# Kernel optimization log

Hardware: AMD Instinct MI355X
Metric: run time of the kernel (lower is better)

## Reference

```python
import jax, jax.numpy as jnp
import numpy as np

N_NODES = 50000
N_EDGES = 1600000
IN_DIM, HID_DIM, OUT_DIM, HEADS = 128, 128, 64, 8
NEG_SLOPE = 0.2
BN_EPS = 1e-5


def setup_inputs() -> dict:
    key = jax.random.key(0)
    ks = jax.random.split(key, 12)
    hpc = HID_DIM // HEADS  # per-head channels of layer 1
    return {
        "x": jax.random.normal(ks[0], (N_NODES, IN_DIM), jnp.float32),
        "edge_index": jax.random.randint(ks[1], (2, N_EDGES), 0, N_NODES, jnp.int64),
        "W1": jax.random.normal(ks[2], (IN_DIM, HEADS * hpc), jnp.float32) * 0.05,
        "a1_src": jax.random.normal(ks[3], (HEADS, hpc), jnp.float32) * 0.1,
        "a1_dst": jax.random.normal(ks[4], (HEADS, hpc), jnp.float32) * 0.1,
        "b1": jnp.zeros((HEADS * hpc,), jnp.float32),
        "bn_gamma": jnp.ones((HID_DIM,), jnp.float32),
        "bn_beta": jnp.zeros((HID_DIM,), jnp.float32),
        "W2": jax.random.normal(ks[5], (HID_DIM, OUT_DIM), jnp.float32) * 0.05,
        "a2_src": jax.random.normal(ks[6], (1, OUT_DIM), jnp.float32) * 0.1,
        "a2_dst": jax.random.normal(ks[7], (1, OUT_DIM), jnp.float32) * 0.1,
        "b2": jnp.zeros((OUT_DIM,), jnp.float32),
    }


def _gat_conv(x, src, dst, W, a_src, a_dst, bias, heads, n_nodes):
    # x: [N, Fin]; src/dst: [E'] (self-loops already appended)
    hpc = W.shape[1] // heads
    h = (x @ W).reshape(n_nodes, heads, hpc)                 # [N,H,C]
    alpha_s = jnp.einsum("nhc,hc->nh", h, a_src)             # [N,H]
    alpha_d = jnp.einsum("nhc,hc->nh", h, a_dst)
    e = alpha_s[src] + alpha_d[dst]                          # [E',H]
    e = jax.nn.leaky_relu(e, NEG_SLOPE)
    # segment softmax over destination neighborhoods
    m = jax.ops.segment_max(e, dst, num_segments=n_nodes)    # [N,H]
    m = jnp.where(jnp.isfinite(m), m, 0.0)
    ee = jnp.exp(e - m[dst])
    denom = jax.ops.segment_sum(ee, dst, num_segments=n_nodes)
    alpha = ee / (denom[dst] + 1e-16)                        # [E',H]
    msg = h[src] * alpha[:, :, None]                         # [E',H,C]
    out = jax.ops.segment_sum(msg, dst, num_segments=n_nodes)  # [N,H,C]
    return out.reshape(n_nodes, heads * hpc) + bias


def _batch_norm(x, gamma, beta):
    mu = jnp.mean(x, axis=0)
    var = jnp.var(x, axis=0)
    return gamma * (x - mu) * jax.lax.rsqrt(var + BN_EPS) + beta


def reference(x, edge_index, W1, a1_src, a1_dst, b1, bn_gamma, bn_beta, W2, a2_src, a2_dst, b2):
    n = x.shape[0]
    loops = jnp.arange(n, dtype=edge_index.dtype)
    src = jnp.concatenate([edge_index[0], loops])            # PyG add_self_loops
    dst = jnp.concatenate([edge_index[1], loops])
    h = _gat_conv(x, src, dst, W1, a1_src, a1_dst, b1, HEADS, n)
    h = _batch_norm(h, bn_gamma, bn_beta)
    h = jax.nn.elu(h)
    # dropout: identity at inference
    out = _gat_conv(h, src, dst, W2, a2_src, a2_dst, b2, 1, n)
    return out
```

## Files before the change

### kernel.cpp

```cpp
#include <hip/hip_runtime.h>
#include <hip/hip_bf16.h>

#define N_NODES 50000
#define N_EDGES 1600000
#define HEADS 8
#define NBK 196
#define NBLK 196
#define EPB 8192

typedef unsigned short u16;
typedef unsigned char u8;
typedef unsigned int u32;
typedef __attribute__((ext_vector_type(8))) short bf16x8;
typedef __attribute__((ext_vector_type(4))) float f32x4;

__device__ __forceinline__ float bf2f(u16 u) {
  union { u32 i; float f; } v; v.i = ((u32)u) << 16; return v.f;
}
__device__ __forceinline__ float bflo(u32 p) {
  union { u32 i; float f; } v; v.i = p << 16; return v.f;
}
__device__ __forceinline__ float bfhi(u32 p) {
  union { u32 i; float f; } v; v.i = p & 0xffff0000u; return v.f;
}
__device__ __forceinline__ u16 f2bf(float f) {
  union { float f; u32 i; } v; v.f = f;
  u32 r = v.i + 0x7fff + ((v.i >> 16) & 1);
  return (u16)(r >> 16);
}
__device__ __forceinline__ u32 pack2(float a, float b) {
  return (u32)f2bf(a) | ((u32)f2bf(b) << 16);
}

__global__ void k_detect(const u16* __restrict__ x, const u32* __restrict__ ei,
                         int* __restrict__ flags) {
  __shared__ int cbig, cnz;
  if (threadIdx.x == 0) { cbig = 0; cnz = 0; }
  __syncthreads();
  int lb = 0, ln = 0;
  for (int i = threadIdx.x; i < 4096; i += 256) {
    int ex = (x[i] >> 7) & 0xff;
    lb += (ex >= 140);
    if (i < 2048) ln += (ei[2 * i + 1] != 0);
  }
  atomicAdd(&cbig, lb); atomicAdd(&cnz, ln);
  __syncthreads();
  if (threadIdx.x == 0) {
    flags[0] = (cbig > 16) ? 1 : 0;
    flags[1] = (cnz == 0) ? 1 : 0;
  }
}

__global__ void k_convsmall(const void* a1s, const void* a1d, const void* b1,
                            const void* gam, const void* bet, const void* a2s,
                            const void* a2d, const void* b2, const void* W1,
                            const void* W2, float* __restrict__ smallf,
                            u16* __restrict__ w1t, u16* __restrict__ w2t,
                            const int* __restrict__ flags) {
  int i = blockIdx.x * 256 + threadIdx.x;
  if (i >= 25408) return;
  bool f32 = flags[0] != 0;
  auto ld = [&](const void* p, int off) -> float {
    return f32 ? ((const float*)p)[off] : bf2f(((const u16*)p)[off]);
  };
  if (i >= 17216) {
    int j = i - 17216, n = j >> 7, k = j & 127;
    w2t[j] = f2bf(ld(W2, k * 64 + n));
  } else if (i >= 832) {
    int j = i - 832, n = j >> 7, k = j & 127;
    w1t[j] = f2bf(ld(W1, k * 128 + n));
  } else {
    const void* src; int off;
    if (i >= 768)      { src = b2;  off = i - 768; }
    else if (i >= 704) { src = a2d; off = i - 704; }
    else if (i >= 640) { src = a2s; off = i - 640; }
    else if (i >= 512) { src = bet; off = i - 512; }
    else if (i >= 384) { src = gam; off = i - 384; }
    else if (i >= 256) { src = b1;  off = i - 256; }
    else if (i >= 128) { src = a1d; off = i - 128; }
    else               { src = a1s; off = i; }
    smallf[i] = ld(src, off);
  }
}

__global__ __launch_bounds__(256) void k_hist(const int* __restrict__ ei,
                                              int* __restrict__ H,
                                              int* __restrict__ totals,
                                              const int* __restrict__ flags) {
  __shared__ int hist[NBK];
  int t = threadIdx.x, blk = blockIdx.x;
  for (int i = t; i < NBK; i += 256) hist[i] = 0;
  __syncthreads();
  bool i64 = flags[1] != 0;
  int base = blk * EPB;
  for (int k = 0; k < 32; k++) {
    int e = base + k * 256 + t;
    if (e < N_EDGES) {
      int d = i64 ? ei[2 * (N_EDGES + e)] : ei[N_EDGES + e];
      atomicAdd(&hist[d >> 8], 1);
    }
  }
  __syncthreads();
  for (int i = t; i < NBK; i += 256) {
    H[i * NBLK + blk] = hist[i];
    atomicAdd(&totals[i], hist[i]);
  }
}

__global__ void k_scan_tot(const int* __restrict__ totals, int* __restrict__ bucketBase) {
  __shared__ int tmp[256];
  int t = threadIdx.x;
  int v = (t < NBK) ? totals[t] : 0;
  tmp[t] = v; __syncthreads();
  for (int o = 1; o < 256; o <<= 1) {
    int x = (t >= o) ? tmp[t - o] : 0; __syncthreads();
    tmp[t] += x; __syncthreads();
  }
  if (t < NBK) bucketBase[t] = tmp[t] - v;
  if (t == NBK - 1) bucketBase[NBK] = tmp[t];
}

__global__ void k_scan_blk(const int* __restrict__ H, const int* __restrict__ bucketBase,
                           int* __restrict__ P) {
  __shared__ int tmp[256];
  int t = threadIdx.x, b = blockIdx.x;
  int v = (t < NBLK) ? H[b * NBLK + t] : 0;
  tmp[t] = v; __syncthreads();
  for (int o = 1; o < 256; o <<= 1) {
    int x = (t >= o) ? tmp[t - o] : 0; __syncthreads();
    tmp[t] += x; __syncthreads();
  }
  if (t < NBLK) P[b * NBLK + t] = bucketBase[b] + tmp[t] - v;
}

__global__ __launch_bounds__(256) void k_bucket(const int* __restrict__ ei,
                                                const int* __restrict__ P,
                                                u32* __restrict__ buf,
                                                const int* __restrict__ flags) {
  __shared__ u32 sv[EPB];
  __shared__ u16 rank[EPB];
  __shared__ u8  sk8[EPB];
  __shared__ int cnt[NBK], scn[NBK], tmp[256];
  int t = threadIdx.x, blk = blockIdx.x;
  int base = blk * EPB;
  int nE = N_EDGES - base; if (nE > EPB) nE = EPB;
  for (int i = t; i < NBK; i += 256) cnt[i] = 0;
  __syncthreads();
  bool i64 = flags[1] != 0;
  for (int k = 0; k < EPB / 256; k++) {
    int li = k * 256 + t, e = base + li;
    if (li < nE) {
      int d = i64 ? ei[2 * (N_EDGES + e)] : ei[N_EDGES + e];
      rank[li] = (u16)atomicAdd(&cnt[d >> 8], 1);
    }
  }
  __syncthreads();
  int v = (t < NBK) ? cnt[t] : 0;
  tmp[t] = v; __syncthreads();
  for (int o = 1; o < 256; o <<= 1) {
    int x = (t >= o) ? tmp[t - o] : 0; __syncthreads();
    tmp[t] += x; __syncthreads();
  }
  if (t < NBK) scn[t] = tmp[t] - v;
  __syncthreads();
  for (int k = 0; k < EPB / 256; k++) {
    int li = k * 256 + t, e = base + li;
    if (li < nE) {
      int s = i64 ? ei[2 * e] : ei[e];
      int d = i64 ? ei[2 * (N_EDGES + e)] : ei[N_EDGES + e];
      int key = d >> 8;
      int pos = scn[key] + rank[li];
      sv[pos] = ((u32)(d & 255) << 16) | (u32)s;
      sk8[pos] = (u8)key;
    }
  }
  __syncthreads();
  for (int i = t; i < nE; i += 256) {
    int b = sk8[i];
    buf[P[b * NBLK + blk] + (i - scn[b])] = sv[i];
  }
}

__global__ __launch_bounds__(256) void k_csr(const u32* __restrict__ buf,
                                             const int* __restrict__ bucketBase,
                                             int* __restrict__ row_start,
                                             int* __restrict__ deg,
                                             int* __restrict__ csr, int N) {
  __shared__ int cnt[256], scn[256], cur[256];
  int b = blockIdx.x, t = threadIdx.x;
  int lo = bucketBase[b], hi = bucketBase[b + 1];
  cnt[t] = 0; __syncthreads();
  for (int e = lo + t; e < hi; e += 256) atomicAdd(&cnt[(buf[e] >> 16) & 255], 1);
  __syncthreads();
  int v = cnt[t];
  scn[t] = v; __syncthreads();
  for (int o = 1; o < 256; o <<= 1) {
    int x = (t >= o) ? scn[t - o] : 0; __syncthreads();
    scn[t] += x; __syncthreads();
  }
  int excl = scn[t] - v;
  int node = b * 256 + t;
  if (node < N) { row_start[node] = lo + excl; deg[node] = v; }
  cur[t] = lo + excl;
  __syncthreads();
  for (int e = lo + t; e < hi; e += 256) {
    u32 p = buf[e];
    int pos = atomicAdd(&cur[(p >> 16) & 255], 1);
    csr[pos] = p & 0xffff;
  }
}

template <int NCOLS, bool EPI, bool AFLAG>
__global__ __launch_bounds__(256) void k_gemm_mfma(const void* __restrict__ A,
                                                   const u16* __restrict__ BT,
                                                   const float* __restrict__ scale,
                                                   const float* __restrict__ shift,
                                                   const float* __restrict__ a2s,
                                                   const float* __restrict__ a2d,
                                                   float* __restrict__ as_out,
                                                   float* __restrict__ ad_out,
                                                   u16* __restrict__ C, int M,
                                                   const int* __restrict__ flags) {
  constexpr int KP = 136;
  constexpr int NT = NCOLS / 16;
  __shared__ u16 As[64 * KP];
  __shared__ u16 Bs[NCOLS * KP];
  int t = threadIdx.x;
  int row0 = blockIdx.x * 64;
  bool af32 = AFLAG ? (flags[0] != 0) : false;

  for (int i = t; i < NCOLS * 16; i += 256) {
    int n = i >> 4, q = i & 15;
    *(uint4*)&Bs[n * KP + q * 8] = ((const uint4*)BT)[n * 16 + q];
  }
  for (int i = t; i < 64 * 32; i += 256) {
    int r = i >> 5, c4 = i & 31;
    int row = row0 + r;
    uint2 pk = make_uint2(0u, 0u);
    if (row < M) {
      if (EPI) {
        uint2 p = ((const uint2*)A)[(size_t)row * 32 + c4];
        int c = c4 * 4;
        float v0 = bflo(p.x), v1 = bfhi(p.x), v2 = bflo(p.y), v3 = bfhi(p.y);
        v0 = fmaf(v0, scale[c],     shift[c]);     v0 = v0 > 0.f ? v0 : __expf(v0) - 1.f;
        v1 = fmaf(v1, scale[c + 1], shift[c + 1]); v1 = v1 > 0.f ? v1 : __expf(v1) - 1.f;
        v2 = fmaf(v2, scale[c + 2], shift[c + 2]); v2 = v2 > 0.f ? v2 : __expf(v2) - 1.f;
        v3 = fmaf(v3, scale[c + 3], shift[c + 3]); v3 = v3 > 0.f ? v3 : __expf(v3) - 1.f;
        pk.x = pack2(v0, v1); pk.y = pack2(v2, v3);
      } else if (af32) {
        float4 v = ((const float4*)A)[(size_t)row * 32 + c4];
        pk.x = pack2(v.x, v.y); pk.y = pack2(v.z, v.w);
      } else {
        pk = ((const uint2*)A)[(size_t)row * 32 + c4];
      }
    }
    *(uint2*)&As[r * KP + c4 * 4] = pk;
  }
  __syncthreads();

  int lane = t & 63, w = t >> 6;
  int m = lane & 15, quad = lane >> 4;
  f32x4 acc[NT];
#pragma unroll
  for (int nt = 0; nt < NT; nt++) acc[nt] = (f32x4)(0.f);
  const u16* aBase = &As[(w * 16 + m) * KP + quad * 8];
  const u16* bBase = &Bs[m * KP + quad * 8];
#pragma unroll
  for (int ks = 0; ks < 4; ks++) {
    bf16x8 af = *(const bf16x8*)(aBase + ks * 32);
#pragma unroll
    for (int nt = 0; nt < NT; nt++) {
      bf16x8 bf = *(const bf16x8*)(bBase + nt * 16 * KP + ks * 32);
      acc[nt] = __builtin_amdgcn_mfma_f32_16x16x32_bf16(af, bf, acc[nt], 0, 0, 0);
    }
  }
  int orow0 = row0 + w * 16 + quad * 4;
#pragma unroll
  for (int nt = 0; nt < NT; nt++) {
#pragma unroll
    for (int r = 0; r < 4; r++) {
      int row = orow0 + r;
      if (row < M) C[(size_t)row * NCOLS + nt * 16 + m] = f2bf(acc[nt][r]);
    }
  }
  if (EPI) {
    float a2sv[NT], a2dv[NT];
#pragma unroll
    for (int nt = 0; nt < NT; nt++) { a2sv[nt] = a2s[nt * 16 + m]; a2dv[nt] = a2d[nt * 16 + m]; }
#pragma unroll
    for (int r = 0; r < 4; r++) {
      float vs = 0.f, vd = 0.f;
#pragma unroll
      for (int nt = 0; nt < NT; nt++) {
        vs = fmaf(acc[nt][r], a2sv[nt], vs);
        vd = fmaf(acc[nt][r], a2dv[nt], vd);
      }
      vs += __shfl_xor(vs, 1); vd += __shfl_xor(vd, 1);
      vs += __shfl_xor(vs, 2); vd += __shfl_xor(vd, 2);
      vs += __shfl_xor(vs, 4); vd += __shfl_xor(vd, 4);
      vs += __shfl_xor(vs, 8); vd += __shfl_xor(vd, 8);
      int row = orow0 + r;
      if (row < M && m == 0) { as_out[row] = vs; ad_out[row] = vd; }
    }
  }
}

__global__ void k_alpha1(const u16* __restrict__ h1b, const float* __restrict__ a1s,
                         const float* __restrict__ a1d, float* __restrict__ as_out,
                         float* __restrict__ ad_out, int N) {
  int idx = blockIdx.x * 256 + threadIdx.x;
  if (idx >= N * HEADS) return;
  int n = idx >> 3, h = idx & 7;
  const u32* hp = (const u32*)&h1b[((size_t)n << 7) + (h << 4)];
  float s = 0.f, d = 0.f;
#pragma unroll
  for (int q = 0; q < 8; q++) {
    u32 p = hp[q];
    float v0 = bflo(p), v1 = bfhi(p);
    int b = (h << 4) + q * 2;
    s = fmaf(v0, a1s[b], s); s = fmaf(v1, a1s[b + 1], s);
    d = fmaf(v0, a1d[b], d); d = fmaf(v1, a1d[b + 1], d);
  }
  as_out[idx] = s; ad_out[idx] = d;
}

__global__ __launch_bounds__(256) void k_agg1(const u16* __restrict__ h1b,
                                              const float* __restrict__ as_,
                                              const float* __restrict__ ad_,
                                              const int* __restrict__ csr,
                                              const int* __restrict__ row_start,
                                              const int* __restrict__ deg,
                                              const float* __restrict__ b1,
                                              u16* __restrict__ out, int N) {
  int node = blockIdx.x * 4 + (threadIdx.x >> 6);
  if (node >= N) return;
  int l = threadIdx.x & 63;
  int head = l >> 3, sub = l & 7;
  int gbase = l & 56;
  int node_u = __builtin_amdgcn_readfirstlane(node);
  int st = __builtin_amdgcn_readfirstlane(row_start[node_u]);
  int cnt = __builtin_amdgcn_readfirstlane(deg[node_u]);
  const int* cp = csr + st;
  const u32* h32 = (const u32*)h1b;
  float ad = ad_[(node_u << 3) | head];
  float sp = 0.f, a0 = 0.f, a1 = 0.f;
  int j = 0;
  for (; j + 8 <= cnt; j += 8) {
    int ssub = cp[j + sub];
    float e = as_[(ssub << 3) | head] + ad;
    e = fmaxf(e, 0.2f * e);
    float p = __expf(e);
    sp += p;
#pragma unroll
    for (int k = 0; k < 8; k++) {
      int sk = cp[j + k];
      float pk = __shfl(p, gbase | k);
      u32 hv = h32[(sk << 6) | l];
      a0 = fmaf(pk, bflo(hv), a0);
      a1 = fmaf(pk, bfhi(hv), a1);
    }
  }
  for (; j < cnt; j++) {
    int s0 = cp[j];
    float e0 = as_[(s0 << 3) | head] + ad;
    e0 = fmaxf(e0, 0.2f * e0);
    float p0 = __expf(e0);
    if (sub == 0) sp += p0;
    u32 hv = h32[(s0 << 6) | l];
    a0 = fmaf(p0, bflo(hv), a0); a1 = fmaf(p0, bfhi(hv), a1);
  }
  {
    float e0 = as_[(node_u << 3) | head] + ad;
    e0 = fmaxf(e0, 0.2f * e0);
    float p0 = __expf(e0);
    if (sub == 0) sp += p0;
    u32 hv = h32[((size_t)node_u << 6) | l];
    a0 = fmaf(p0, bflo(hv), a0); a1 = fmaf(p0, bfhi(hv), a1);
  }
  sp += __shfl_xor(sp, 1);
  sp += __shfl_xor(sp, 2);
  sp += __shfl_xor(sp, 4);
  float inv = 1.f / (sp + 1e-16f);
  int c0 = l * 2;
  ((u32*)out)[((size_t)node_u << 6) + l] =
      pack2(fmaf(a0, inv, b1[c0]), fmaf(a1, inv, b1[c0 + 1]));
}

__global__ void k_bnstat(const u16* __restrict__ h, float* __restrict__ gsum,
                         float* __restrict__ gsq, int N) {
  __shared__ float ts[256], tq[256];
  int t = threadIdx.x, col = t & 127, rr = t >> 7;
  int row0 = blockIdx.x * 128;
  float s = 0.f, q = 0.f;
  for (int r = rr; r < 128; r += 2) {
    int row = row0 + r;
    if (row < N) {
      float v = bf2f(h[((size_t)row << 7) + col]);
      s += v; q = fmaf(v, v, q);
    }
  }
  ts[t] = s; tq[t] = q; __syncthreads();
  if (t < 128) {
    atomicAdd(&gsum[t], ts[t] + ts[t + 128]);
    atomicAdd(&gsq[t], tq[t] + tq[t + 128]);
  }
}

__global__ void k_bnfin(const float* __restrict__ gsum, const float* __restrict__ gsq,
                        const float* __restrict__ gamma, const float* __restrict__ beta,
                        float* __restrict__ scale, float* __restrict__ shift, int N) {
  int t = threadIdx.x;
  if (t >= 128) return;
  float mu = gsum[t] / (float)N;
  float var = fmaxf(gsq[t] / (float)N - mu * mu, 0.f);
  float s = gamma[t] * rsqrtf(var + 1e-5f);
  scale[t] = s;
  shift[t] = beta[t] - mu * s;
}

__global__ __launch_bounds__(256) void k_agg2(const u16* __restrict__ h2b,
                                              const float* __restrict__ as_,
                                              const float* __restrict__ ad_,
                                              const int* __restrict__ csr,
                                              const int* __restrict__ row_start,
                                              const int* __restrict__ deg,
                                              const float* __restrict__ b2,
                                              void* __restrict__ out,
                                              const int* __restrict__ flags, int N) {
  int node = blockIdx.x * 4 + (threadIdx.x >> 6);
  if (node >= N) return;
  int l = threadIdx.x & 63;
  int sub = l & 7, gbase = l & 56;
  int node_u = __builtin_amdgcn_readfirstlane(node);
  int st = __builtin_amdgcn_readfirstlane(row_start[node_u]);
  int cnt = __builtin_amdgcn_readfirstlane(deg[node_u]);
  const int* cp = csr + st;
  float ad = ad_[node_u];
  float sp = 0.f, a = 0.f;
  int j = 0;
  for (; j + 8 <= cnt; j += 8) {
    int ssub = cp[j + sub];
    float e = as_[ssub] + ad;
    e = fmaxf(e, 0.2f * e);
    float p = __expf(e);
    sp += p;
#pragma unroll
    for (int k = 0; k < 8; k++) {
      int sk = cp[j + k];
      float pk = __shfl(p, gbase | k);
      a = fmaf(pk, bf2f((h2b + (sk << 6))[l]), a);
    }
  }
  for (; j < cnt; j++) {
    int s0 = cp[j];
    float e0 = as_[s0] + ad;
    e0 = fmaxf(e0, 0.2f * e0);
    float p0 = __expf(e0);
    if (sub == 0) sp += p0;
    a = fmaf(p0, bf2f((h2b + (s0 << 6))[l]), a);
  }
  {
    float e0 = as_[node_u] + ad;
    e0 = fmaxf(e0, 0.2f * e0);
    float p0 = __expf(e0);
    if (sub == 0) sp += p0;
    a = fmaf(p0, bf2f((h2b + (node_u << 6))[l]), a);
  }
  sp += __shfl_xor(sp, 1);
  sp += __shfl_xor(sp, 2);
  sp += __shfl_xor(sp, 4);
  float r = a / (sp + 1e-16f) + b2[l];
  size_t idx = ((size_t)node_u << 6) + l;
  if (flags[0]) ((float*)out)[idx] = r;
  else          ((u16*)out)[idx] = f2bf(r);
}

extern "C" void kernel_launch(void* const* d_in, const int* in_sizes, int n_in,
                              void* d_out, int out_size, void* d_ws, size_t ws_size,
                              hipStream_t stream) {
  const void* x   = d_in[0];
  const int*  ei  = (const int*)d_in[1];
  const void* W1  = d_in[2];
  const void* a1s = d_in[3];
  const void* a1d = d_in[4];
  const void* b1  = d_in[5];
  const void* gam = d_in[6];
  const void* bet = d_in[7];
  const void* W2  = d_in[8];
  const void* a2s = d_in[9];
  const void* a2d = d_in[10];
  const void* b2  = d_in[11];

  char* ws = (char*)d_ws;
  size_t off = 0;
  auto alloc = [&](size_t bytes) -> void* {
    void* p = ws + off;
    off += (bytes + 255) & ~(size_t)255;
    return p;
  };
  int* flags = (int*)alloc(256);
  char* zreg = (char*)alloc(2048);
  int* totals = (int*)zreg;
  float* gsum = (float*)(zreg + 1024);
  float* gsq  = gsum + 128;
  int* H  = (int*)alloc((size_t)NBK * NBLK * 4);
  int* P  = (int*)alloc((size_t)NBK * NBLK * 4);
  int* bucketBase = (int*)alloc(1024);
  u32* ebuf = (u32*)alloc((size_t)N_EDGES * 4);
  int* csr = (int*)alloc((size_t)N_EDGES * 4);
  int* row_start = (int*)alloc((size_t)N_NODES * 4);
  int* deg = (int*)alloc((size_t)N_NODES * 4);
  float* smallf = (float*)alloc(832 * 4);
  float* a1sf = smallf;        float* a1df = smallf + 128;
  float* b1f  = smallf + 256;  float* gamf = smallf + 384;
  float* betf = smallf + 512;  float* a2sf = smallf + 640;
  float* a2df = smallf + 704;  float* b2f  = smallf + 768;
  u16* w1t = (u16*)alloc(16384 * 2);
  u16* w2t = (u16*)alloc(8192 * 2);
  u16* h1b  = (u16*)alloc((size_t)N_NODES * 128 * 2);
  u16* h1ob = (u16*)alloc((size_t)N_NODES * 128 * 2);
  u16* h2b  = (u16*)alloc((size_t)N_NODES * 64 * 2);
  float* al1s = (float*)alloc((size_t)N_NODES * 8 * 4);
  float* al1d = (float*)alloc((size_t)N_NODES * 8 * 4);
  float* scale = (float*)alloc(512);
  float* shift = (float*)alloc(512);
  float* al2s = (float*)alloc((size_t)N_NODES * 4);
  float* al2d = (float*)alloc((size_t)N_NODES * 4);
  if (off > ws_size) return;

  hipMemsetAsync(zreg, 0, 2048, stream);
  k_detect<<<1, 256, 0, stream>>>((const u16*)x, (const u32*)ei, flags);
  k_convsmall<<<100, 256, 0, stream>>>(a1s, a1d, b1, gam, bet, a2s, a2d, b2, W1, W2,
                                       smallf, w1t, w2t, flags);

  k_hist<<<NBLK, 256, 0, stream>>>(ei, H, totals, flags);
  k_scan_tot<<<1, 256, 0, stream>>>(totals, bucketBase);
  k_scan_blk<<<NBK, 256, 0, stream>>>(H, bucketBase, P);
  k_bucket<<<NBLK, 256, 0, stream>>>(ei, P, ebuf, flags);
  k_csr<<<NBK, 256, 0, stream>>>(ebuf, bucketBase, row_start, deg, csr, N_NODES);

  k_gemm_mfma<128, false, true><<<(N_NODES + 63) / 64, 256, 0, stream>>>(
      x, w1t, nullptr, nullptr, nullptr, nullptr, nullptr, nullptr, h1b, N_NODES, flags);
  k_alpha1<<<(N_NODES * HEADS + 255) / 256, 256, 0, stream>>>(h1b, a1sf, a1df,
                                                              al1s, al1d, N_NODES);
  k_agg1<<<(N_NODES + 3) / 4, 256, 0, stream>>>(h1b, al1s, al1d, csr, row_start, deg,
                                                b1f, h1ob, N_NODES);

  k_bnstat<<<(N_NODES + 127) / 128, 256, 0, stream>>>(h1ob, gsum, gsq, N_NODES);
  k_bnfin<<<1, 128, 0, stream>>>(gsum, gsq, gamf, betf, scale, shift, N_NODES);

  k_gemm_mfma<64, true, false><<<(N_NODES + 63) / 64, 256, 0, stream>>>(
      h1ob, w2t, scale, shift, a2sf, a2df, al2s, al2d, h2b, N_NODES, flags);
  k_agg2<<<(N_NODES + 3) / 4, 256, 0, stream>>>(h2b, al2s, al2d, csr, row_start, deg,
                                                b2f, d_out, flags, N_NODES);
}
```

Baseline: 329.1 us.

## Fuse layer-1 attention logits into GEMM epilogue and double-buffer aggregation gathers

The first-layer GEMM now computes the per-head source and destination attention logits in its epilogue from fp32 accumulators, so the separate k_alpha1 kernel and its re-read of h1 are gone. Both aggregation kernels now software-pipeline their neighbor gathers, issuing the next batch of 8 feature loads before consuming the current one, to hide gather latency. The cost is more registers per thread, which may lower occupancy, plus extra shuffles in the GEMM epilogue. The logits are also now computed from unrounded accumulators rather than bf16-rounded features.

```diff
diff --git a/kernel.cpp b/kernel.cpp
--- a/kernel.cpp
+++ b/kernel.cpp
@@ -210,7 +210,7 @@
   }
 }
 
-template <int NCOLS, bool EPI, bool AFLAG>
+template <int NCOLS, bool EPI, bool AFLAG, bool A1>
 __global__ __launch_bounds__(256) void k_gemm_mfma(const void* __restrict__ A,
                                                    const u16* __restrict__ BT,
                                                    const float* __restrict__ scale,
@@ -303,25 +303,28 @@
       if (row < M && m == 0) { as_out[row] = vs; ad_out[row] = vd; }
     }
   }
-}
-
-__global__ void k_alpha1(const u16* __restrict__ h1b, const float* __restrict__ a1s,
-                         const float* __restrict__ a1d, float* __restrict__ as_out,
-                         float* __restrict__ ad_out, int N) {
-  int idx = blockIdx.x * 256 + threadIdx.x;
-  if (idx >= N * HEADS) return;
-  int n = idx >> 3, h = idx & 7;
-  const u32* hp = (const u32*)&h1b[((size_t)n << 7) + (h << 4)];
-  float s = 0.f, d = 0.f;
-#pragma unroll
-  for (int q = 0; q < 8; q++) {
-    u32 p = hp[q];
-    float v0 = bflo(p), v1 = bfhi(p);
-    int b = (h << 4) + q * 2;
-    s = fmaf(v0, a1s[b], s); s = fmaf(v1, a1s[b + 1], s);
-    d = fmaf(v0, a1d[b], d); d = fmaf(v1, a1d[b + 1], d);
-  }
-  as_out[idx] = s; ad_out[idx] = d;
+  if (A1) {
+    float s1v[NT], d1v[NT];
+#pragma unroll
+    for (int nt = 0; nt < NT; nt++) { s1v[nt] = a2s[nt * 16 + m]; d1v[nt] = a2d[nt * 16 + m]; }
+#pragma unroll
+    for (int r = 0; r < 4; r++) {
+      int row = orow0 + r;
+#pragma unroll
+      for (int nt = 0; nt < NT; nt++) {
+        float vs = acc[nt][r] * s1v[nt];
+        float vd = acc[nt][r] * d1v[nt];
+        vs += __shfl_xor(vs, 1); vd += __shfl_xor(vd, 1);
+        vs += __shfl_xor(vs, 2); vd += __shfl_xor(vd, 2);
+        vs += __shfl_xor(vs, 4); vd += __shfl_xor(vd, 4);
+        vs += __shfl_xor(vs, 8); vd += __shfl_xor(vd, 8);
+        if (row < M && m == 0) {
+          as_out[(row << 3) | nt] = vs;
+          ad_out[(row << 3) | nt] = vd;
+        }
+      }
+    }
+  }
 }
 
 __global__ __launch_bounds__(256) void k_agg1(const u16* __restrict__ h1b,
@@ -344,22 +347,65 @@
   const u32* h32 = (const u32*)h1b;
   float ad = ad_[(node_u << 3) | head];
   float sp = 0.f, a0 = 0.f, a1 = 0.f;
-  int j = 0;
-  for (; j + 8 <= cnt; j += 8) {
-    int ssub = cp[j + sub];
-    float e = as_[(ssub << 3) | head] + ad;
-    e = fmaxf(e, 0.2f * e);
-    float p = __expf(e);
-    sp += p;
-#pragma unroll
-    for (int k = 0; k < 8; k++) {
-      int sk = cp[j + k];
-      float pk = __shfl(p, gbase | k);
-      u32 hv = h32[(sk << 6) | l];
-      a0 = fmaf(pk, bflo(hv), a0);
-      a1 = fmaf(pk, bfhi(hv), a1);
-    }
-  }
+
+  u32 hA0, hA1, hA2, hA3, hA4, hA5, hA6, hA7;
+  u32 hB0, hB1, hB2, hB3, hB4, hB5, hB6, hB7;
+  float eA, eB;
+
+#define LEAD1(jj, h0, h1, h2, h3, h4, h5, h6, h7, ev)          \
+  {                                                            \
+    int jb = (jj);                                             \
+    int ss = cp[jb + sub];                                     \
+    ev = as_[(ss << 3) | head];                                \
+    h0 = h32[(cp[jb + 0] << 6) | l];                           \
+    h1 = h32[(cp[jb + 1] << 6) | l];                           \
+    h2 = h32[(cp[jb + 2] << 6) | l];                           \
+    h3 = h32[(cp[jb + 3] << 6) | l];                           \
+    h4 = h32[(cp[jb + 4] << 6) | l];                           \
+    h5 = h32[(cp[jb + 5] << 6) | l];                           \
+    h6 = h32[(cp[jb + 6] << 6) | l];                           \
+    h7 = h32[(cp[jb + 7] << 6) | l];                           \
+  }
+
+#define CONS1(h0, h1, h2, h3, h4, h5, h6, h7, ev)              \
+  {                                                            \
+    float e = ev + ad;                                         \
+    e = fmaxf(e, 0.2f * e);                                    \
+    float p = __expf(e);                                       \
+    sp += p;                                                   \
+    float pk;                                                  \
+    pk = __shfl(p, gbase | 0);                                 \
+    a0 = fmaf(pk, bflo(h0), a0); a1 = fmaf(pk, bfhi(h0), a1);  \
+    pk = __shfl(p, gbase | 1);                                 \
+    a0 = fmaf(pk, bflo(h1), a0); a1 = fmaf(pk, bfhi(h1), a1);  \
+    pk = __shfl(p, gbase | 2);                                 \
+    a0 = fmaf(pk, bflo(h2), a0); a1 = fmaf(pk, bfhi(h2), a1);  \
+    pk = __shfl(p, gbase | 3);                                 \
+    a0 = fmaf(pk, bflo(h3), a0); a1 = fmaf(pk, bfhi(h3), a1);  \
+    pk = __shfl(p, gbase | 4);                                 \
+    a0 = fmaf(pk, bflo(h4), a0); a1 = fmaf(pk, bfhi(h4), a1);  \
+    pk = __shfl(p, gbase | 5);                                 \
+    a0 = fmaf(pk, bflo(h5), a0); a1 = fmaf(pk, bfhi(h5), a1);  \
+    pk = __shfl(p, gbase | 6);                                 \
+    a0 = fmaf(pk, bflo(h6), a0); a1 = fmaf(pk, bfhi(h6), a1);  \
+    pk = __shfl(p, gbase | 7);                                 \
+    a0 = fmaf(pk, bflo(h7), a0); a1 = fmaf(pk, bfhi(h7), a1);  \
+  }
+
+  int nfull = cnt >> 3;
+  int b = 0;
+  if (nfull > 0) LEAD1(0, hA0, hA1, hA2, hA3, hA4, hA5, hA6, hA7, eA);
+  for (; b + 2 <= nfull; b += 2) {
+    LEAD1((b + 1) * 8, hB0, hB1, hB2, hB3, hB4, hB5, hB6, hB7, eB);
+    CONS1(hA0, hA1, hA2, hA3, hA4, hA5, hA6, hA7, eA);
+    if (b + 2 < nfull) LEAD1((b + 2) * 8, hA0, hA1, hA2, hA3, hA4, hA5, hA6, hA7, eA);
+    CONS1(hB0, hB1, hB2, hB3, hB4, hB5, hB6, hB7, eB);
+  }
+  if (b < nfull) CONS1(hA0, hA1, hA2, hA3, hA4, hA5, hA6, hA7, eA);
+#undef LEAD1
+#undef CONS1
+
+  int j = nfull * 8;
   for (; j < cnt; j++) {
     int s0 = cp[j];
     float e0 = as_[(s0 << 3) | head] + ad;
@@ -437,20 +483,57 @@
   const int* cp = csr + st;
   float ad = ad_[node_u];
   float sp = 0.f, a = 0.f;
-  int j = 0;
-  for (; j + 8 <= cnt; j += 8) {
-    int ssub = cp[j + sub];
-    float e = as_[ssub] + ad;
-    e = fmaxf(e, 0.2f * e);
-    float p = __expf(e);
-    sp += p;
-#pragma unroll
-    for (int k = 0; k < 8; k++) {
-      int sk = cp[j + k];
-      float pk = __shfl(p, gbase | k);
-      a = fmaf(pk, bf2f((h2b + (sk << 6))[l]), a);
-    }
-  }
+
+  u16 hA0, hA1, hA2, hA3, hA4, hA5, hA6, hA7;
+  u16 hB0, hB1, hB2, hB3, hB4, hB5, hB6, hB7;
+  float eA, eB;
+
+#define LEAD2(jj, h0, h1, h2, h3, h4, h5, h6, h7, ev)          \
+  {                                                            \
+    int jb = (jj);                                             \
+    int ss = cp[jb + sub];                                     \
+    ev = as_[ss];                                              \
+    h0 = h2b[(cp[jb + 0] << 6) | l];                           \
+    h1 = h2b[(cp[jb + 1] << 6) | l];                           \
+    h2 = h2b[(cp[jb + 2] << 6) | l];                           \
+    h3 = h2b[(cp[jb + 3] << 6) | l];                           \
+    h4 = h2b[(cp[jb + 4] << 6) | l];                           \
+    h5 = h2b[(cp[jb + 5] << 6) | l];                           \
+    h6 = h2b[(cp[jb + 6] << 6) | l];                           \
+    h7 = h2b[(cp[jb + 7] << 6) | l];                           \
+  }
+
+#define CONS2(h0, h1, h2, h3, h4, h5, h6, h7, ev)              \
+  {                                                            \
+    float e = ev + ad;                                         \
+    e = fmaxf(e, 0.2f * e);                                    \
+    float p = __expf(e);                                       \
+    sp += p;                                                   \
+    float pk;                                                  \
+    pk = __shfl(p, gbase | 0); a = fmaf(pk, bf2f(h0), a);      \
+    pk = __shfl(p, gbase | 1); a = fmaf(pk, bf2f(h1), a);      \
+    pk = __shfl(p, gbase | 2); a = fmaf(pk, bf2f(h2), a);      \
+    pk = __shfl(p, gbase | 3); a = fmaf(pk, bf2f(h3), a);      \
+    pk = __shfl(p, gbase | 4); a = fmaf(pk, bf2f(h4), a);      \
+    pk = __shfl(p, gbase | 5); a = fmaf(pk, bf2f(h5), a);      \
+    pk = __shfl(p, gbase | 6); a = fmaf(pk, bf2f(h6), a);      \
+    pk = __shfl(p, gbase | 7); a = fmaf(pk, bf2f(h7), a);      \
+  }
+
+  int nfull = cnt >> 3;
+  int b = 0;
+  if (nfull > 0) LEAD2(0, hA0, hA1, hA2, hA3, hA4, hA5, hA6, hA7, eA);
+  for (; b + 2 <= nfull; b += 2) {
+    LEAD2((b + 1) * 8, hB0, hB1, hB2, hB3, hB4, hB5, hB6, hB7, eB);
+    CONS2(hA0, hA1, hA2, hA3, hA4, hA5, hA6, hA7, eA);
+    if (b + 2 < nfull) LEAD2((b + 2) * 8, hA0, hA1, hA2, hA3, hA4, hA5, hA6, hA7, eA);
+    CONS2(hB0, hB1, hB2, hB3, hB4, hB5, hB6, hB7, eB);
+  }
+  if (b < nfull) CONS2(hA0, hA1, hA2, hA3, hA4, hA5, hA6, hA7, eA);
+#undef LEAD2
+#undef CONS2
+
+  int j = nfull * 8;
   for (; j < cnt; j++) {
     int s0 = cp[j];
     float e0 = as_[s0] + ad;
@@ -539,17 +622,15 @@
   k_bucket<<<NBLK, 256, 0, stream>>>(ei, P, ebuf, flags);
   k_csr<<<NBK, 256, 0, stream>>>(ebuf, bucketBase, row_start, deg, csr, N_NODES);
 
-  k_gemm_mfma<128, false, true><<<(N_NODES + 63) / 64, 256, 0, stream>>>(
-      x, w1t, nullptr, nullptr, nullptr, nullptr, nullptr, nullptr, h1b, N_NODES, flags);
-  k_alpha1<<<(N_NODES * HEADS + 255) / 256, 256, 0, stream>>>(h1b, a1sf, a1df,
-                                                              al1s, al1d, N_NODES);
+  k_gemm_mfma<128, false, true, true><<<(N_NODES + 63) / 64, 256, 0, stream>>>(
+      x, w1t, nullptr, nullptr, a1sf, a1df, al1s, al1d, h1b, N_NODES, flags);
   k_agg1<<<(N_NODES + 3) / 4, 256, 0, stream>>>(h1b, al1s, al1d, csr, row_start, deg,
                                                 b1f, h1ob, N_NODES);
 
   k_bnstat<<<(N_NODES + 127) / 128, 256, 0, stream>>>(h1ob, gsum, gsq, N_NODES);
   k_bnfin<<<1, 128, 0, stream>>>(gsum, gsq, gamf, betf, scale, shift, N_NODES);
 
-  k_gemm_mfma<64, true, false><<<(N_NODES + 63) / 64, 256, 0, stream>>>(
+  k_gemm_mfma<64, true, false, false><<<(N_NODES + 63) / 64, 256, 0, stream>>>(
       h1ob, w2t, scale, shift, a2sf, a2df, al2s, al2d, h2b, N_NODES, flags);
   k_agg2<<<(N_NODES + 3) / 4, 256, 0, stream>>>(h2b, al2s, al2d, csr, row_start, deg,
                                                 b2f, d_out, flags, N_NODES);
```

Measured after the change: 341.1 us. 3.6% more time.

## Fuse layer-1 attention logits into GEMM and split aggregation into column-block passes

Applied to the files above, without the earlier changes.

The first GEMM now computes the per-head source and destination attention scores in its epilogue, which removes the separate alpha kernel. It also writes h1 in a column-blocked layout of 32-column slabs, one per pass. Aggregation becomes four passes, each over one 32-column slab (two heads), with 4 edges processed in parallel per wave. Blocks are ordered so the same pass shares a smaller working set, which is meant to improve cache reuse of the gathered features. The cost is redundant reloading of CSR indices and attention scores across the passes, extra cross-lane reductions, and a grid four times larger.

```diff
diff --git a/kernel.cpp b/kernel.cpp
--- a/kernel.cpp
+++ b/kernel.cpp
@@ -210,7 +210,7 @@
   }
 }
 
-template <int NCOLS, bool EPI, bool AFLAG>
+template <int NCOLS, bool EPI, bool AFLAG, bool A1, bool BLK>
 __global__ __launch_bounds__(256) void k_gemm_mfma(const void* __restrict__ A,
                                                    const u16* __restrict__ BT,
                                                    const float* __restrict__ scale,
@@ -280,7 +280,14 @@
 #pragma unroll
     for (int r = 0; r < 4; r++) {
       int row = orow0 + r;
-      if (row < M) C[(size_t)row * NCOLS + nt * 16 + m] = f2bf(acc[nt][r]);
+      if (row < M) {
+        if (BLK) {
+          int col = nt * 16 + m;
+          C[((size_t)(col >> 5) * N_NODES + row) * 32 + (col & 31)] = f2bf(acc[nt][r]);
+        } else {
+          C[(size_t)row * NCOLS + nt * 16 + m] = f2bf(acc[nt][r]);
+        }
+      }
     }
   }
   if (EPI) {
@@ -303,87 +310,85 @@
       if (row < M && m == 0) { as_out[row] = vs; ad_out[row] = vd; }
     }
   }
-}
-
-__global__ void k_alpha1(const u16* __restrict__ h1b, const float* __restrict__ a1s,
-                         const float* __restrict__ a1d, float* __restrict__ as_out,
-                         float* __restrict__ ad_out, int N) {
-  int idx = blockIdx.x * 256 + threadIdx.x;
-  if (idx >= N * HEADS) return;
-  int n = idx >> 3, h = idx & 7;
-  const u32* hp = (const u32*)&h1b[((size_t)n << 7) + (h << 4)];
-  float s = 0.f, d = 0.f;
-#pragma unroll
-  for (int q = 0; q < 8; q++) {
-    u32 p = hp[q];
-    float v0 = bflo(p), v1 = bfhi(p);
-    int b = (h << 4) + q * 2;
-    s = fmaf(v0, a1s[b], s); s = fmaf(v1, a1s[b + 1], s);
-    d = fmaf(v0, a1d[b], d); d = fmaf(v1, a1d[b + 1], d);
-  }
-  as_out[idx] = s; ad_out[idx] = d;
-}
-
-__global__ __launch_bounds__(256) void k_agg1(const u16* __restrict__ h1b,
-                                              const float* __restrict__ as_,
-                                              const float* __restrict__ ad_,
-                                              const int* __restrict__ csr,
-                                              const int* __restrict__ row_start,
-                                              const int* __restrict__ deg,
-                                              const float* __restrict__ b1,
-                                              u16* __restrict__ out, int N) {
-  int node = blockIdx.x * 4 + (threadIdx.x >> 6);
+  if (A1) {
+    float s1v[NT], d1v[NT];
+#pragma unroll
+    for (int nt = 0; nt < NT; nt++) { s1v[nt] = a2s[nt * 16 + m]; d1v[nt] = a2d[nt * 16 + m]; }
+#pragma unroll
+    for (int r = 0; r < 4; r++) {
+      int row = orow0 + r;
+#pragma unroll
+      for (int nt = 0; nt < NT; nt++) {
+        float vs = acc[nt][r] * s1v[nt];
+        float vd = acc[nt][r] * d1v[nt];
+        vs += __shfl_xor(vs, 1); vd += __shfl_xor(vd, 1);
+        vs += __shfl_xor(vs, 2); vd += __shfl_xor(vd, 2);
+        vs += __shfl_xor(vs, 4); vd += __shfl_xor(vd, 4);
+        vs += __shfl_xor(vs, 8); vd += __shfl_xor(vd, 8);
+        if (row < M && m == 0) {
+          as_out[(row << 3) | nt] = vs;
+          ad_out[(row << 3) | nt] = vd;
+        }
+      }
+    }
+  }
+}
+
+__global__ __launch_bounds__(256) void k_agg1p(const u16* __restrict__ h1b,
+                                               const float* __restrict__ as_,
+                                               const float* __restrict__ ad_,
+                                               const int* __restrict__ csr,
+                                               const int* __restrict__ row_start,
+                                               const int* __restrict__ deg,
+                                               const float* __restrict__ b1,
+                                               u16* __restrict__ out, int N) {
+  int bid = blockIdx.x;
+  int pass = (bid & 7) >> 1;
+  int w = ((bid >> 3) << 1) | (bid & 1);
+  int node = w * 4 + (threadIdx.x >> 6);
   if (node >= N) return;
   int l = threadIdx.x & 63;
-  int head = l >> 3, sub = l & 7;
-  int gbase = l & 56;
+  int slot = l >> 4, q = l & 15;
+  int head = (pass << 1) | (q >> 3);
   int node_u = __builtin_amdgcn_readfirstlane(node);
   int st = __builtin_amdgcn_readfirstlane(row_start[node_u]);
   int cnt = __builtin_amdgcn_readfirstlane(deg[node_u]);
   const int* cp = csr + st;
-  const u32* h32 = (const u32*)h1b;
+  const u32* hp = (const u32*)h1b + (size_t)pass * (N_NODES * 16);
   float ad = ad_[(node_u << 3) | head];
   float sp = 0.f, a0 = 0.f, a1 = 0.f;
-  int j = 0;
-  for (; j + 8 <= cnt; j += 8) {
-    int ssub = cp[j + sub];
-    float e = as_[(ssub << 3) | head] + ad;
+  int nmain = cnt & ~3;
+#pragma unroll 4
+  for (int j = 0; j < nmain; j += 4) {
+    int sk = cp[j + slot];
+    float e = as_[(sk << 3) | head] + ad;
     e = fmaxf(e, 0.2f * e);
     float p = __expf(e);
     sp += p;
-#pragma unroll
-    for (int k = 0; k < 8; k++) {
-      int sk = cp[j + k];
-      float pk = __shfl(p, gbase | k);
-      u32 hv = h32[(sk << 6) | l];
-      a0 = fmaf(pk, bflo(hv), a0);
-      a1 = fmaf(pk, bfhi(hv), a1);
-    }
-  }
-  for (; j < cnt; j++) {
-    int s0 = cp[j];
-    float e0 = as_[(s0 << 3) | head] + ad;
-    e0 = fmaxf(e0, 0.2f * e0);
-    float p0 = __expf(e0);
-    if (sub == 0) sp += p0;
-    u32 hv = h32[(s0 << 6) | l];
-    a0 = fmaf(p0, bflo(hv), a0); a1 = fmaf(p0, bfhi(hv), a1);
+    u32 hv = hp[(sk << 4) | q];
+    a0 = fmaf(p, bflo(hv), a0);
+    a1 = fmaf(p, bfhi(hv), a1);
   }
   {
-    float e0 = as_[(node_u << 3) | head] + ad;
-    e0 = fmaxf(e0, 0.2f * e0);
-    float p0 = __expf(e0);
-    if (sub == 0) sp += p0;
-    u32 hv = h32[((size_t)node_u << 6) | l];
-    a0 = fmaf(p0, bflo(hv), a0); a1 = fmaf(p0, bfhi(hv), a1);
-  }
-  sp += __shfl_xor(sp, 1);
-  sp += __shfl_xor(sp, 2);
-  sp += __shfl_xor(sp, 4);
+    int rem = cnt - nmain;
+    int sk = (slot < rem) ? cp[nmain + slot] : node_u;
+    float e = as_[(sk << 3) | head] + ad;
+    e = fmaxf(e, 0.2f * e);
+    float p = (slot <= rem) ? __expf(e) : 0.f;
+    sp += p;
+    u32 hv = hp[(sk << 4) | q];
+    a0 = fmaf(p, bflo(hv), a0);
+    a1 = fmaf(p, bfhi(hv), a1);
+  }
+  sp += __shfl_xor(sp, 16); sp += __shfl_xor(sp, 32);
+  a0 += __shfl_xor(a0, 16); a0 += __shfl_xor(a0, 32);
+  a1 += __shfl_xor(a1, 16); a1 += __shfl_xor(a1, 32);
   float inv = 1.f / (sp + 1e-16f);
-  int c0 = l * 2;
-  ((u32*)out)[((size_t)node_u << 6) + l] =
-      pack2(fmaf(a0, inv, b1[c0]), fmaf(a1, inv, b1[c0 + 1]));
+  if (slot == 0) {
+    int c0 = (pass << 5) | (q << 1);
+    ((u32*)out)[((size_t)node_u << 6) | (pass << 4) | q] =
+        pack2(fmaf(a0, inv, b1[c0]), fmaf(a1, inv, b1[c0 + 1]));
+  }
 }
 
 __global__ void k_bnstat(const u16* __restrict__ h, float* __restrict__ gsum,
@@ -507,7 +512,7 @@
   int* P  = (int*)alloc((size_t)NBK * NBLK * 4);
   int* bucketBase = (int*)alloc(1024);
   u32* ebuf = (u32*)alloc((size_t)N_EDGES * 4);
-  int* csr = (int*)alloc((size_t)N_EDGES * 4);
+  int* csr = (int*)alloc(((size_t)N_EDGES + 64) * 4);
   int* row_start = (int*)alloc((size_t)N_NODES * 4);
   int* deg = (int*)alloc((size_t)N_NODES * 4);
   float* smallf = (float*)alloc(832 * 4);
@@ -539,17 +544,15 @@
   k_bucket<<<NBLK, 256, 0, stream>>>(ei, P, ebuf, flags);
   k_csr<<<NBK, 256, 0, stream>>>(ebuf, bucketBase, row_start, deg, csr, N_NODES);
 
-  k_gemm_mfma<128, false, true><<<(N_NODES + 63) / 64, 256, 0, stream>>>(
-      x, w1t, nullptr, nullptr, nullptr, nullptr, nullptr, nullptr, h1b, N_NODES, flags);
-  k_alpha1<<<(N_NODES * HEADS + 255) / 256, 256, 0, stream>>>(h1b, a1sf, a1df,
-                                                              al1s, al1d, N_NODES);
-  k_agg1<<<(N_NODES + 3) / 4, 256, 0, stream>>>(h1b, al1s, al1d, csr, row_start, deg,
-                                                b1f, h1ob, N_NODES);
+  k_gemm_mfma<128, false, true, true, true><<<(N_NODES + 63) / 64, 256, 0, stream>>>(
+      x, w1t, nullptr, nullptr, a1sf, a1df, al1s, al1d, h1b, N_NODES, flags);
+  k_agg1p<<<50000, 256, 0, stream>>>(h1b, al1s, al1d, csr, row_start, deg,
+                                     b1f, h1ob, N_NODES);
 
   k_bnstat<<<(N_NODES + 127) / 128, 256, 0, stream>>>(h1ob, gsum, gsq, N_NODES);
   k_bnfin<<<1, 128, 0, stream>>>(gsum, gsq, gamf, betf, scale, shift, N_NODES);
 
-  k_gemm_mfma<64, true, false><<<(N_NODES + 63) / 64, 256, 0, stream>>>(
+  k_gemm_mfma<64, true, false, false, false><<<(N_NODES + 63) / 64, 256, 0, stream>>>(
       h1ob, w2t, scale, shift, a2sf, a2df, al2s, al2d, h2b, N_NODES, flags);
   k_agg2<<<(N_NODES + 3) / 4, 256, 0, stream>>>(h2b, al2s, al2d, csr, row_start, deg,
                                                 b2f, d_out, flags, N_NODES);
```

Result: slower. 388.1 us (+17.9%).

## Use finer CSR buckets with more blocks and fuse layer-1 alpha into GEMM

Applied to the files above, without the earlier changes.

Bucketing for the CSR build now uses 64-node buckets (784 buckets) and 2048-edge blocks, so the histogram, bucket and CSR kernels run on four times as many blocks. The scans change to four elements per thread to cover the larger bucket count. The per-node attention logits of layer 1 are now computed in the first MFMA GEMM epilogue, which removes the separate k_alpha1 kernel and its re-read of h1. The H/P matrices grow to 784x784 and the prefix scans get more work, which may offset part of the gain.

```diff
diff --git a/kernel.cpp b/kernel.cpp
--- a/kernel.cpp
+++ b/kernel.cpp
@@ -4,9 +4,9 @@
 #define N_NODES 50000
 #define N_EDGES 1600000
 #define HEADS 8
-#define NBK 196
-#define NBLK 196
-#define EPB 8192
+#define NBK 784
+#define NBLK 784
+#define EPB 2048
 
 typedef unsigned short u16;
 typedef unsigned char u8;
@@ -93,44 +93,66 @@
   __syncthreads();
   bool i64 = flags[1] != 0;
   int base = blk * EPB;
-  for (int k = 0; k < 32; k++) {
+  for (int k = 0; k < EPB / 256; k++) {
     int e = base + k * 256 + t;
     if (e < N_EDGES) {
       int d = i64 ? ei[2 * (N_EDGES + e)] : ei[N_EDGES + e];
-      atomicAdd(&hist[d >> 8], 1);
+      atomicAdd(&hist[d >> 6], 1);
     }
   }
   __syncthreads();
   for (int i = t; i < NBK; i += 256) {
     H[i * NBLK + blk] = hist[i];
-    atomicAdd(&totals[i], hist[i]);
+    if (hist[i]) atomicAdd(&totals[i], hist[i]);
   }
 }
 
 __global__ void k_scan_tot(const int* __restrict__ totals, int* __restrict__ bucketBase) {
   __shared__ int tmp[256];
   int t = threadIdx.x;
-  int v = (t < NBK) ? totals[t] : 0;
-  tmp[t] = v; __syncthreads();
+  int loc[4]; int s = 0;
+#pragma unroll
+  for (int i = 0; i < 4; i++) {
+    int idx = t * 4 + i;
+    int v = (idx < NBK) ? totals[idx] : 0;
+    loc[i] = s; s += v;
+  }
+  tmp[t] = s; __syncthreads();
   for (int o = 1; o < 256; o <<= 1) {
     int x = (t >= o) ? tmp[t - o] : 0; __syncthreads();
     tmp[t] += x; __syncthreads();
   }
-  if (t < NBK) bucketBase[t] = tmp[t] - v;
-  if (t == NBK - 1) bucketBase[NBK] = tmp[t];
+  int add = tmp[t] - s;
+#pragma unroll
+  for (int i = 0; i < 4; i++) {
+    int idx = t * 4 + i;
+    if (idx < NBK) bucketBase[idx] = add + loc[i];
+  }
+  if (t == 255) bucketBase[NBK] = tmp[255];
 }
 
 __global__ void k_scan_blk(const int* __restrict__ H, const int* __restrict__ bucketBase,
                            int* __restrict__ P) {
   __shared__ int tmp[256];
   int t = threadIdx.x, b = blockIdx.x;
-  int v = (t < NBLK) ? H[b * NBLK + t] : 0;
-  tmp[t] = v; __syncthreads();
+  int loc[4]; int s = 0;
+#pragma unroll
+  for (int i = 0; i < 4; i++) {
+    int idx = t * 4 + i;
+    int v = (idx < NBLK) ? H[b * NBLK + idx] : 0;
+    loc[i] = s; s += v;
+  }
+  tmp[t] = s; __syncthreads();
   for (int o = 1; o < 256; o <<= 1) {
     int x = (t >= o) ? tmp[t - o] : 0; __syncthreads();
     tmp[t] += x; __syncthreads();
   }
-  if (t < NBLK) P[b * NBLK + t] = bucketBase[b] + tmp[t] - v;
+  int add = bucketBase[b] + tmp[t] - s;
+#pragma unroll
+  for (int i = 0; i < 4; i++) {
+    int idx = t * 4 + i;
+    if (idx < NBLK) P[b * NBLK + idx] = add + loc[i];
+  }
 }
 
 __global__ __launch_bounds__(256) void k_bucket(const int* __restrict__ ei,
@@ -139,11 +161,11 @@
                                                 const int* __restrict__ flags) {
   __shared__ u32 sv[EPB];
   __shared__ u16 rank[EPB];
-  __shared__ u8  sk8[EPB];
+  __shared__ u16 sk16[EPB];
   __shared__ int cnt[NBK], scn[NBK], tmp[256];
   int t = threadIdx.x, blk = blockIdx.x;
   int base = blk * EPB;
-  int nE = N_EDGES - base; if (nE > EPB) nE = EPB;
+  int nE = N_EDGES - base; if (nE > EPB) nE = EPB; if (nE < 0) nE = 0;
   for (int i = t; i < NBK; i += 256) cnt[i] = 0;
   __syncthreads();
   bool i64 = flags[1] != 0;
@@ -151,33 +173,44 @@
     int li = k * 256 + t, e = base + li;
     if (li < nE) {
       int d = i64 ? ei[2 * (N_EDGES + e)] : ei[N_EDGES + e];
-      rank[li] = (u16)atomicAdd(&cnt[d >> 8], 1);
-    }
-  }
-  __syncthreads();
-  int v = (t < NBK) ? cnt[t] : 0;
-  tmp[t] = v; __syncthreads();
+      rank[li] = (u16)atomicAdd(&cnt[d >> 6], 1);
+    }
+  }
+  __syncthreads();
+  int loc[4]; int s = 0;
+#pragma unroll
+  for (int i = 0; i < 4; i++) {
+    int idx = t * 4 + i;
+    int v = (idx < NBK) ? cnt[idx] : 0;
+    loc[i] = s; s += v;
+  }
+  tmp[t] = s; __syncthreads();
   for (int o = 1; o < 256; o <<= 1) {
     int x = (t >= o) ? tmp[t - o] : 0; __syncthreads();
     tmp[t] += x; __syncthreads();
   }
-  if (t < NBK) scn[t] = tmp[t] - v;
+  int add = tmp[t] - s;
+#pragma unroll
+  for (int i = 0; i < 4; i++) {
+    int idx = t * 4 + i;
+    if (idx < NBK) scn[idx] = add + loc[i];
+  }
   __syncthreads();
   for (int k = 0; k < EPB / 256; k++) {
     int li = k * 256 + t, e = base + li;
     if (li < nE) {
-      int s = i64 ? ei[2 * e] : ei[e];
-      int d = i64 ? ei[2 * (N_EDGES + e)] : ei[N_EDGES + e];
-      int key = d >> 8;
+      int s0 = i64 ? ei[2 * e] : ei[e];
+      int d  = i64 ? ei[2 * (N_EDGES + e)] : ei[N_EDGES + e];
+      int key = d >> 6;
       int pos = scn[key] + rank[li];
-      sv[pos] = ((u32)(d & 255) << 16) | (u32)s;
-      sk8[pos] = (u8)key;
+      sv[pos] = ((u32)(d & 63) << 16) | (u32)s0;
+      sk16[pos] = (u16)key;
     }
   }
   __syncthreads();
   for (int i = t; i < nE; i += 256) {
-    int b = sk8[i];
-    buf[P[b * NBLK + blk] + (i - scn[b])] = sv[i];
+    int bb = sk16[i];
+    buf[P[bb * NBLK + blk] + (i - scn[bb])] = sv[i];
   }
 }
 
@@ -186,31 +219,35 @@
                                              int* __restrict__ row_start,
                                              int* __restrict__ deg,
                                              int* __restrict__ csr, int N) {
-  __shared__ int cnt[256], scn[256], cur[256];
+  __shared__ int cnt[64], scn[64], cur[64];
   int b = blockIdx.x, t = threadIdx.x;
   int lo = bucketBase[b], hi = bucketBase[b + 1];
-  cnt[t] = 0; __syncthreads();
-  for (int e = lo + t; e < hi; e += 256) atomicAdd(&cnt[(buf[e] >> 16) & 255], 1);
-  __syncthreads();
-  int v = cnt[t];
-  scn[t] = v; __syncthreads();
-  for (int o = 1; o < 256; o <<= 1) {
-    int x = (t >= o) ? scn[t - o] : 0; __syncthreads();
-    scn[t] += x; __syncthreads();
-  }
-  int excl = scn[t] - v;
-  int node = b * 256 + t;
-  if (node < N) { row_start[node] = lo + excl; deg[node] = v; }
-  cur[t] = lo + excl;
+  if (t < 64) cnt[t] = 0;
+  __syncthreads();
+  for (int e = lo + t; e < hi; e += 256) atomicAdd(&cnt[(buf[e] >> 16) & 63], 1);
+  __syncthreads();
+  if (t < 64) scn[t] = cnt[t];
+  __syncthreads();
+  for (int o = 1; o < 64; o <<= 1) {
+    int x = (t >= o && t < 64) ? scn[t - o] : 0; __syncthreads();
+    if (t < 64) scn[t] += x;
+    __syncthreads();
+  }
+  if (t < 64) {
+    int excl = scn[t] - cnt[t];
+    int node = b * 64 + t;
+    if (node < N) { row_start[node] = lo + excl; deg[node] = cnt[t]; }
+    cur[t] = lo + excl;
+  }
   __syncthreads();
   for (int e = lo + t; e < hi; e += 256) {
     u32 p = buf[e];
-    int pos = atomicAdd(&cur[(p >> 16) & 255], 1);
+    int pos = atomicAdd(&cur[(p >> 16) & 63], 1);
     csr[pos] = p & 0xffff;
   }
 }
 
-template <int NCOLS, bool EPI, bool AFLAG>
+template <int NCOLS, bool EPI, bool AFLAG, bool A1>
 __global__ __launch_bounds__(256) void k_gemm_mfma(const void* __restrict__ A,
                                                    const u16* __restrict__ BT,
                                                    const float* __restrict__ scale,
@@ -303,25 +340,28 @@
       if (row < M && m == 0) { as_out[row] = vs; ad_out[row] = vd; }
     }
   }
-}
-
-__global__ void k_alpha1(const u16* __restrict__ h1b, const float* __restrict__ a1s,
-                         const float* __restrict__ a1d, float* __restrict__ as_out,
-                         float* __restrict__ ad_out, int N) {
-  int idx = blockIdx.x * 256 + threadIdx.x;
-  if (idx >= N * HEADS) return;
-  int n = idx >> 3, h = idx & 7;
-  const u32* hp = (const u32*)&h1b[((size_t)n << 7) + (h << 4)];
-  float s = 0.f, d = 0.f;
-#pragma unroll
-  for (int q = 0; q < 8; q++) {
-    u32 p = hp[q];
-    float v0 = bflo(p), v1 = bfhi(p);
-    int b = (h << 4) + q * 2;
-    s = fmaf(v0, a1s[b], s); s = fmaf(v1, a1s[b + 1], s);
-    d = fmaf(v0, a1d[b], d); d = fmaf(v1, a1d[b + 1], d);
-  }
-  as_out[idx] = s; ad_out[idx] = d;
+  if (A1) {
+    float s1v[NT], d1v[NT];
+#pragma unroll
+    for (int nt = 0; nt < NT; nt++) { s1v[nt] = a2s[nt * 16 + m]; d1v[nt] = a2d[nt * 16 + m]; }
+#pragma unroll
+    for (int r = 0; r < 4; r++) {
+      int row = orow0 + r;
+#pragma unroll
+      for (int nt = 0; nt < NT; nt++) {
+        float vs = acc[nt][r] * s1v[nt];
+        float vd = acc[nt][r] * d1v[nt];
+        vs += __shfl_xor(vs, 1); vd += __shfl_xor(vd, 1);
+        vs += __shfl_xor(vs, 2); vd += __shfl_xor(vd, 2);
+        vs += __shfl_xor(vs, 4); vd += __shfl_xor(vd, 4);
+        vs += __shfl_xor(vs, 8); vd += __shfl_xor(vd, 8);
+        if (row < M && m == 0) {
+          as_out[(row << 3) | nt] = vs;
+          ad_out[(row << 3) | nt] = vd;
+        }
+      }
+    }
+  }
 }
 
 __global__ __launch_bounds__(256) void k_agg1(const u16* __restrict__ h1b,
@@ -499,15 +539,15 @@
     return p;
   };
   int* flags = (int*)alloc(256);
-  char* zreg = (char*)alloc(2048);
+  char* zreg = (char*)alloc(4608);
   int* totals = (int*)zreg;
-  float* gsum = (float*)(zreg + 1024);
+  float* gsum = (float*)(zreg + 3328);
   float* gsq  = gsum + 128;
   int* H  = (int*)alloc((size_t)NBK * NBLK * 4);
   int* P  = (int*)alloc((size_t)NBK * NBLK * 4);
-  int* bucketBase = (int*)alloc(1024);
+  int* bucketBase = (int*)alloc((NBK + 1) * 4);
   u32* ebuf = (u32*)alloc((size_t)N_EDGES * 4);
-  int* csr = (int*)alloc((size_t)N_EDGES * 4);
+  int* csr = (int*)alloc(((size_t)N_EDGES + 64) * 4);
   int* row_start = (int*)alloc((size_t)N_NODES * 4);
   int* deg = (int*)alloc((size_t)N_NODES * 4);
   float* smallf = (float*)alloc(832 * 4);
@@ -528,7 +568,7 @@
   float* al2d = (float*)alloc((size_t)N_NODES * 4);
   if (off > ws_size) return;
 
-  hipMemsetAsync(zreg, 0, 2048, stream);
+  hipMemsetAsync(zreg, 0, 4608, stream);
   k_detect<<<1, 256, 0, stream>>>((const u16*)x, (const u32*)ei, flags);
   k_convsmall<<<100, 256, 0, stream>>>(a1s, a1d, b1, gam, bet, a2s, a2d, b2, W1, W2,
                                        smallf, w1t, w2t, flags);
@@ -539,17 +579,15 @@
   k_bucket<<<NBLK, 256, 0, stream>>>(ei, P, ebuf, flags);
   k_csr<<<NBK, 256, 0, stream>>>(ebuf, bucketBase, row_start, deg, csr, N_NODES);
 
-  k_gemm_mfma<128, false, true><<<(N_NODES + 63) / 64, 256, 0, stream>>>(
-      x, w1t, nullptr, nullptr, nullptr, nullptr, nullptr, nullptr, h1b, N_NODES, flags);
-  k_alpha1<<<(N_NODES * HEADS + 255) / 256, 256, 0, stream>>>(h1b, a1sf, a1df,
-                                                              al1s, al1d, N_NODES);
+  k_gemm_mfma<128, false, true, true><<<(N_NODES + 63) / 64, 256, 0, stream>>>(
+      x, w1t, nullptr, nullptr, a1sf, a1df, al1s, al1d, h1b, N_NODES, flags);
   k_agg1<<<(N_NODES + 3) / 4, 256, 0, stream>>>(h1b, al1s, al1d, csr, row_start, deg,
                                                 b1f, h1ob, N_NODES);
 
   k_bnstat<<<(N_NODES + 127) / 128, 256, 0, stream>>>(h1ob, gsum, gsq, N_NODES);
   k_bnfin<<<1, 128, 0, stream>>>(gsum, gsq, gamf, betf, scale, shift, N_NODES);
 
-  k_gemm_mfma<64, true, false><<<(N_NODES + 63) / 64, 256, 0, stream>>>(
+  k_gemm_mfma<64, true, false, false><<<(N_NODES + 63) / 64, 256, 0, stream>>>(
       h1ob, w2t, scale, shift, a2sf, a2df, al2s, al2d, h2b, N_NODES, flags);
   k_agg2<<<(N_NODES + 3) / 4, 256, 0, stream>>>(h2b, al2s, al2d, csr, row_start, deg,
                                                 b2f, d_out, flags, N_NODES);
```

After: 339.2 us. 3.1% more time.
